# Optimization experiments

Measured on AMD Instinct MI355X. Metric: run time of the kernel, lower is better.

## Reference

```python
import jax, jax.numpy as jnp
import numpy as np

B, L, W, C = 16, 200, 64, 128
H_INTRA = 64   # intra_hidden // 2 per direction
H_INTER = 128
EPS = 1e-8


def layer_norm(x, gamma, beta):
    mu = jnp.mean(x, axis=-1, keepdims=True)
    var = jnp.mean(jnp.square(x - mu), axis=-1, keepdims=True)
    return (x - mu) * jax.lax.rsqrt(var + EPS) * gamma + beta


def gru_seq(x, Wk, Uk, b, H):
    """Keras GRU, reset_after=False, recurrent_activation=sigmoid. x: [N,T,D] -> [N,T,H]."""
    xw = jnp.einsum('ntd,dk->ntk', x, Wk) + b  # precompute input projections [N,T,3H]
    def step(h, xw_t):
        z = jax.nn.sigmoid(xw_t[:, :H] + h @ Uk[:, :H])
        r = jax.nn.sigmoid(xw_t[:, H:2 * H] + h @ Uk[:, H:2 * H])
        hh = jnp.tanh(xw_t[:, 2 * H:] + (r * h) @ Uk[:, 2 * H:])
        h = z * h + (1.0 - z) * hh
        return h, h
    h0 = jnp.zeros((x.shape[0], H), x.dtype)
    _, ys = jax.lax.scan(step, h0, jnp.swapaxes(xw, 0, 1))  # [T,N,H]
    return jnp.swapaxes(ys, 0, 1)


def skip_gru_seq(x, Wk, Uk, b, Wp, bp, H):
    """Skip-RNN GRU (Campos et al.): binary update gate u_t conditionally updates state.
    Returns (outputs [N,T,H], gates [N,T,1])."""
    xw = jnp.einsum('ntd,dk->ntk', x, Wk) + b
    def step(carry, xw_t):
        h, ut = carry
        # straight-through binarization of cumulative update prob
        u = ut + jax.lax.stop_gradient(jnp.round(ut) - ut)  # [N,1]
        z = jax.nn.sigmoid(xw_t[:, :H] + h @ Uk[:, :H])
        r = jax.nn.sigmoid(xw_t[:, H:2 * H] + h @ Uk[:, H:2 * H])
        hh = jnp.tanh(xw_t[:, 2 * H:] + (r * h) @ Uk[:, 2 * H:])
        h_new = z * h + (1.0 - z) * hh
        h = u * h_new + (1.0 - u) * h  # skip: copy state when u == 0
        delta = jax.nn.sigmoid(h @ Wp + bp)  # [N,1]
        ut_next = u * delta + (1.0 - u) * (ut + jnp.minimum(delta, 1.0 - ut))
        return (h, ut_next), (h, u)
    N = x.shape[0]
    h0 = jnp.zeros((N, H), x.dtype)
    ut0 = jnp.ones((N, 1), x.dtype)
    _, (ys, us) = jax.lax.scan(step, (h0, ut0), jnp.swapaxes(xw, 0, 1))
    return jnp.swapaxes(ys, 0, 1), jnp.swapaxes(us, 0, 1)


def setup_inputs():
    key = jax.random.key(0)
    ks = jax.random.split(key, 16)
    rn = lambda k, s: jax.random.normal(k, s, dtype=jnp.float32) * 0.05
    z = lambda s: jnp.zeros(s, jnp.float32)
    o = lambda s: jnp.ones(s, jnp.float32)
    return {
        'x': jax.random.normal(ks[0], (B, L, W, C), dtype=jnp.float32),
        'scale': jax.random.uniform(ks[1], (B, L, W, 1), dtype=jnp.float32),
        'Wf': rn(ks[2], (C, 3 * H_INTRA)), 'Uf': rn(ks[3], (H_INTRA, 3 * H_INTRA)), 'bf': z((3 * H_INTRA,)),
        'Wb': rn(ks[4], (C, 3 * H_INTRA)), 'Ub': rn(ks[5], (H_INTRA, 3 * H_INTRA)), 'bb': z((3 * H_INTRA,)),
        'W_intra_fc': rn(ks[6], (2 * H_INTRA, C)), 'b_intra_fc': z((C,)),
        'g_intra': o((C,)), 'beta_intra': z((C,)),
        'Wi': rn(ks[7], (C + 1, 3 * H_INTER)), 'Ui': rn(ks[8], (H_INTER, 3 * H_INTER)), 'bi': z((3 * H_INTER,)),
        'Wp': rn(ks[9], (H_INTER, 1)), 'bp': z((1,)),
        'W_inter_fc': rn(ks[10], (H_INTER, C)), 'b_inter_fc': z((C,)),
        'g_inter': o((C,)), 'beta_inter': z((C,)),
    }


def reference(x, scale, Wf, Uf, bf, Wb, Ub, bb, W_intra_fc, b_intra_fc, g_intra, beta_intra,
              Wi, Ui, bi, Wp, bp, W_inter_fc, b_inter_fc, g_inter, beta_inter):
    # ----- intra path: bidirectional GRU over the width axis -----
    intra_in = x.reshape(B * L, W, C)
    out_f = gru_seq(intra_in, Wf, Uf, bf, H_INTRA)
    out_b = gru_seq(intra_in[:, ::-1, :], Wb, Ub, bb, H_INTRA)[:, ::-1, :]
    intra_rnn_out = jnp.concatenate([out_f, out_b], axis=-1)  # [B*L, W, 2H]
    update_gate_intra = jnp.ones((64, L), jnp.float32)  # skip=0 branch: constant ones
    intra_dense = intra_rnn_out @ W_intra_fc + b_intra_fc  # [B*L, W, C]
    intra_out = x + layer_norm(intra_dense.reshape(B, L, W, C), g_intra, beta_intra)
    # ----- inter path: skip-GRU over the L (time) axis -----
    inter_in = jnp.transpose(intra_out, (0, 2, 1, 3)).reshape(B * W, L, C)
    scale2 = jnp.transpose(scale, (0, 2, 1, 3)).reshape(B * W, L, 1)
    inter_in = jnp.concatenate([inter_in, scale2], axis=-1)  # [B*W, L, C+1]
    inter_rnn_out, gates = skip_gru_seq(inter_in, Wi, Ui, bi, Wp, bp, H_INTER)
    update_gate_inter = gates[:, :, 0]  # [B*W, L]
    inter_dense = (inter_rnn_out @ W_inter_fc + b_inter_fc).reshape(B, W, L, C)
    inter_ln_in = jnp.transpose(inter_dense, (0, 2, 1, 3))  # [B, L, W, C]
    inter_out = intra_out + layer_norm(inter_ln_in, g_inter, beta_inter)
    return inter_out, update_gate_intra, update_gate_inter
```

## Files before the change

### kernel.cpp

```cpp
#include <hip/hip_runtime.h>
#include <cmath>


typedef float f32x16 __attribute__((ext_vector_type(16)));

__device__ __forceinline__ float sigf(float x) { return 1.0f / (1.0f + expf(-x)); }
__device__ __forceinline__ float rlanef(float v, int l) {
  return __uint_as_float(__builtin_amdgcn_readlane(__float_as_uint(v), (unsigned)l));
}
__device__ __forceinline__ void ldsbar() {
  asm volatile("s_waitcnt lgkmcnt(0)" ::: "memory");
  __builtin_amdgcn_s_barrier();
  __builtin_amdgcn_sched_barrier(0);
}

template <int SB>
__device__ __forceinline__ void macP2(const f32x16& u0, const f32x16& u1, float hv,
                                      float& a0, float& a1) {
#pragma unroll
  for (int k = 0; k < 16; ++k) {
    const float hs = rlanef(hv, SB + k);
    a0 = fmaf(u0[k], hs, a0);
    a1 = fmaf(u1[k], hs, a1);
  }
}
template <int SB>
__device__ __forceinline__ void macP1(const f32x16& u, float hv, float& a) {
#pragma unroll
  for (int k = 0; k < 16; ++k) a = fmaf(u[k], rlanef(hv, SB + k), a);
}

__global__ __launch_bounds__(256) void k_fill_ones(float* __restrict__ p, int n) {
  int i = blockIdx.x * 256 + threadIdx.x;
  if (i < n) p[i] = 1.0f;
}

enum { MA_X_FWD = 0, MA_X_BWD = 1, MA_INTER = 2 };

template <int MODE>
__global__ __launch_bounds__(256) void k_gemm_xw(
    const float* __restrict__ A0, const float* __restrict__ A1,
    const float* __restrict__ Bm, const float* __restrict__ bias,
    float* __restrict__ Cm, long M0, int N, int K, int KT)
{
  __shared__ float As[16][68];
  __shared__ float Bs[16][68];
  const int tid = threadIdx.x;
  const int tx = tid & 15, ty = tid >> 4;
  const long row0g = M0 + (long)blockIdx.x * 64;
  const int col0 = blockIdx.y * 64;
  const int lr = tid >> 2;
  const int lk4 = (tid & 3) * 4;
  const int bk = tid >> 4;
  const int bc4 = (tid & 15) * 4;
  float acc[4][4];
#pragma unroll
  for (int i = 0; i < 4; ++i)
#pragma unroll
    for (int j = 0; j < 4; ++j) acc[i][j] = 0.f;

  for (int kt = 0; kt < KT; ++kt) {
    const int k0 = kt * 16;
    {
      const long rg = row0g + lr;
      float v0, v1, v2, v3;
      if (MODE == MA_X_FWD) {
        const float4 a4 = *reinterpret_cast<const float4*>(&A0[rg * 128 + k0 + lk4]);
        v0 = a4.x; v1 = a4.y; v2 = a4.z; v3 = a4.w;
      } else if (MODE == MA_X_BWD) {
        const long s = rg >> 6; const int t = (int)(rg & 63);
        const float4 a4 =
            *reinterpret_cast<const float4*>(&A0[(s * 64 + (63 - t)) * 128 + k0 + lk4]);
        v0 = a4.x; v1 = a4.y; v2 = a4.z; v3 = a4.w;
      } else {
        const int n = (int)(rg & 1023);
        const int l = (int)(rg >> 10);
        const long rowc = ((long)(n >> 6) * 200 + l) * 64 + (n & 63);
        const long base = rowc * 128;
        if (kt < 8) {
          const float4 a4 = *reinterpret_cast<const float4*>(&A0[base + k0 + lk4]);
          v0 = a4.x; v1 = a4.y; v2 = a4.z; v3 = a4.w;
        } else {
          v0 = (lk4 == 0) ? A1[rowc] : 0.f;
          v1 = 0.f; v2 = 0.f; v3 = 0.f;
        }
      }
      As[lk4 + 0][lr] = v0;
      As[lk4 + 1][lr] = v1;
      As[lk4 + 2][lr] = v2;
      As[lk4 + 3][lr] = v3;
    }
    {
      const int k = k0 + bk;
      float4 b4 = make_float4(0.f, 0.f, 0.f, 0.f);
      if (k < K) b4 = *reinterpret_cast<const float4*>(&Bm[(long)k * N + col0 + bc4]);
      *reinterpret_cast<float4*>(&Bs[bk][bc4]) = b4;
    }
    __syncthreads();
#pragma unroll
    for (int kk = 0; kk < 16; ++kk) {
      const float4 a4 = *reinterpret_cast<const float4*>(&As[kk][ty * 4]);
      const float4 b4 = *reinterpret_cast<const float4*>(&Bs[kk][tx * 4]);
      const float av[4] = {a4.x, a4.y, a4.z, a4.w};
      const float bv[4] = {b4.x, b4.y, b4.z, b4.w};
#pragma unroll
      for (int i = 0; i < 4; ++i)
#pragma unroll
        for (int j = 0; j < 4; ++j) acc[i][j] = fmaf(av[i], bv[j], acc[i][j]);
    }
    __syncthreads();
  }
  const float4 bi4 = *reinterpret_cast<const float4*>(&bias[col0 + tx * 4]);
  const float bv[4] = {bi4.x, bi4.y, bi4.z, bi4.w};
#pragma unroll
  for (int i = 0; i < 4; ++i) {
    const long rl = (long)blockIdx.x * 64 + ty * 4 + i;
    float4 o;
    o.x = acc[i][0] + bv[0];
    o.y = acc[i][1] + bv[1];
    o.z = acc[i][2] + bv[2];
    o.w = acc[i][3] + bv[3];
    *reinterpret_cast<float4*>(&Cm[rl * (long)N + col0 + tx * 4]) = o;
  }
}

__global__ __attribute__((amdgpu_waves_per_eu(4, 4))) __launch_bounds__(256)
void k_gru_intra5(
    const float* __restrict__ xwf, const float* __restrict__ xwb,
    const float* __restrict__ Uf, const float* __restrict__ Ub,
    float* __restrict__ rnn)
{
  const int dir = blockIdx.y;
  const float* __restrict__ xw = dir ? xwb : xwf;
  const float* __restrict__ U  = dir ? Ub : Uf;
  __shared__ float h8[4][64], z8[4][64], rh8[4][64];
  __shared__ float pA[4][4][128];
  __shared__ float pB[4][4][64];
  const int tid = threadIdx.x;
  const int w = tid >> 6, lane = tid & 63;
  const long s0 = (long)blockIdx.x * 4;

  f32x16 uz, ur, uhh;
#pragma unroll
  for (int k = 0; k < 16; ++k) {
    const int row = (w * 16 + k) * 192;
    uz[k]  = U[row + lane];
    ur[k]  = U[row + 64 + lane];
    uhh[k] = U[row + 128 + lane];
  }
  h8[w][lane] = 0.f;
  __syncthreads();

  const long xrow0 = (s0 + w) * 64;
  float xa1 = xw[xrow0 * 192 + lane];
  float xa2 = xw[xrow0 * 192 + 64 + lane];
  float xb  = xw[xrow0 * 192 + 128 + lane];

  for (int t = 0; t < 64; ++t) {
    const int tn = (t < 63) ? t + 1 : t;
    const float xa1n = xw[(xrow0 + tn) * 192 + lane];
    const float xa2n = xw[(xrow0 + tn) * 192 + 64 + lane];
    const float xbn  = xw[(xrow0 + tn) * 192 + 128 + lane];
    {
      const float hv01 = h8[lane >> 5][w * 16 + (lane & 15)];
      const float hv23 = h8[2 + (lane >> 5)][w * 16 + (lane & 15)];
      float az0 = 0.f, ar0 = 0.f, az1 = 0.f, ar1 = 0.f;
      float az2 = 0.f, ar2 = 0.f, az3 = 0.f, ar3 = 0.f;
      macP2<0>(uz, ur, hv01, az0, ar0);
      macP2<32>(uz, ur, hv01, az1, ar1);
      macP2<0>(uz, ur, hv23, az2, ar2);
      macP2<32>(uz, ur, hv23, az3, ar3);
      pA[0][w][lane] = az0; pA[0][w][64 + lane] = ar0;
      pA[1][w][lane] = az1; pA[1][w][64 + lane] = ar1;
      pA[2][w][lane] = az2; pA[2][w][64 + lane] = ar2;
      pA[3][w][lane] = az3; pA[3][w][64 + lane] = ar3;
    }
    ldsbar();
    {
      const float sz = pA[w][0][lane] + pA[w][1][lane] + pA[w][2][lane] +
                       pA[w][3][lane] + xa1;
      const float sr = pA[w][0][64 + lane] + pA[w][1][64 + lane] +
                       pA[w][2][64 + lane] + pA[w][3][64 + lane] + xa2;
      z8[w][lane] = sigf(sz);
      rh8[w][lane] = sigf(sr) * h8[w][lane];
    }
    ldsbar();
    {
      const float rv01 = rh8[lane >> 5][w * 16 + (lane & 15)];
      const float rv23 = rh8[2 + (lane >> 5)][w * 16 + (lane & 15)];
      float a0 = 0.f, a1 = 0.f, a2 = 0.f, a3 = 0.f;
      macP1<0>(uhh, rv01, a0);
      macP1<32>(uhh, rv01, a1);
      macP1<0>(uhh, rv23, a2);
      macP1<32>(uhh, rv23, a3);
      pB[0][w][lane] = a0;
      pB[1][w][lane] = a1;
      pB[2][w][lane] = a2;
      pB[3][w][lane] = a3;
    }
    ldsbar();
    {
      const float pre = pB[w][0][lane] + pB[w][1][lane] + pB[w][2][lane] +
                        pB[w][3][lane] + xb;
      const float hh = tanhf(pre);
      const float z = z8[w][lane];
      const float ho = h8[w][lane];
      const float hn = z * ho + (1.f - z) * hh;
      h8[w][lane] = hn;
      const int tt = dir ? (63 - t) : t;
      rnn[((s0 + w) * 64 + tt) * 128 + dir * 64 + lane] = hn;
    }
    ldsbar();
    xa1 = xa1n; xa2 = xa2n; xb = xbn;
  }
}

__global__ __attribute__((amdgpu_waves_per_eu(4, 4))) __launch_bounds__(512)
void k_gru_inter8(
    const float* __restrict__ xw, const float* __restrict__ Ui,
    const float* __restrict__ Wp, const float* __restrict__ bp,
    float* __restrict__ rnn, float* __restrict__ gates,
    float* __restrict__ hstate, float* __restrict__ ustate,
    int t0, int nt)
{
  __shared__ float h4[2][128], z4[2][128], rh4[2][128];
  __shared__ float pA[2][8][256];
  __shared__ float pB[2][8][128];
  __shared__ float uu[2], utt[2];
  const int tid = threadIdx.x;
  const int w = tid >> 6, lane = tid & 63;
  const int kb = w << 4;
  const int n0 = blockIdx.x * 2;

  f32x16 u0, u1, u2, u3;
  f32x16 v0, v1;
#pragma unroll
  for (int k = 0; k < 16; ++k) {
    const long r = (long)(kb + k) * 384;
    u0[k] = Ui[r + lane];
    u1[k] = Ui[r + 64 + lane];
    u2[k] = Ui[r + 128 + lane];
    u3[k] = Ui[r + 192 + lane];
    v0[k] = Ui[r + 256 + lane];
    v1[k] = Ui[r + 320 + lane];
  }
  if (tid < 256) {
    const int s = tid >> 7, c = tid & 127;
    h4[s][c] = (t0 == 0) ? 0.f : hstate[(long)(n0 + s) * 128 + c];
  }
  if (tid < 2) {
    utt[tid] = (t0 == 0) ? 1.f : ustate[n0 + tid];
    uu[tid]  = (t0 == 0) ? 1.f : ustate[1024 + n0 + tid];
  }
  const float bp0 = bp[0];
  float wpA = 0.f, wpB = 0.f;
  if (w < 2) { wpA = Wp[lane]; wpB = Wp[64 + lane]; }
  __syncthreads();

  const int sC = tid >> 8;
  const int cC = tid & 255;

  for (int dl = 0; dl < nt; ++dl) {
    const float u0g = uu[0], u1g = uu[1];
    const bool act = (u0g + u1g) != 0.f;
    if (act) {
      const float xc = xw[((long)dl * 1024 + n0 + sC) * 384 + cC];
      float xbA = 0.f, xbB = 0.f;
      if (w < 2) {
        xbA = xw[((long)dl * 1024 + n0 + w) * 384 + 256 + lane];
        xbB = xw[((long)dl * 1024 + n0 + w) * 384 + 320 + lane];
      }
      {
        if (u0g != 0.f) {
          const float hv = h4[0][kb + (lane & 15)];
          float a0 = 0.f, a1 = 0.f, a2 = 0.f, a3 = 0.f;
#pragma unroll
          for (int j = 0; j < 16; ++j) {
            const float hs = rlanef(hv, j);
            a0 = fmaf(u0[j], hs, a0);
            a1 = fmaf(u1[j], hs, a1);
            a2 = fmaf(u2[j], hs, a2);
            a3 = fmaf(u3[j], hs, a3);
          }
          pA[0][w][lane] = a0; pA[0][w][64 + lane] = a1;
          pA[0][w][128 + lane] = a2; pA[0][w][192 + lane] = a3;
        }
        if (u1g != 0.f) {
          const float hv = h4[1][kb + (lane & 15)];
          float a0 = 0.f, a1 = 0.f, a2 = 0.f, a3 = 0.f;
#pragma unroll
          for (int j = 0; j < 16; ++j) {
            const float hs = rlanef(hv, j);
            a0 = fmaf(u0[j], hs, a0);
            a1 = fmaf(u1[j], hs, a1);
            a2 = fmaf(u2[j], hs, a2);
            a3 = fmaf(u3[j], hs, a3);
          }
          pA[1][w][lane] = a0; pA[1][w][64 + lane] = a1;
          pA[1][w][128 + lane] = a2; pA[1][w][192 + lane] = a3;
        }
      }
      ldsbar();
      {
        if (uu[sC] != 0.f) {
          float sum = xc;
#pragma unroll
          for (int q = 0; q < 8; ++q) sum += pA[sC][q][cC];
          if (cC < 128) z4[sC][cC] = sigf(sum);
          else rh4[sC][cC - 128] = sigf(sum) * h4[sC][cC - 128];
        }
      }
      ldsbar();
      {
        if (u0g != 0.f) {
          const float rv = rh4[0][kb + (lane & 15)];
          float b0 = 0.f, b1 = 0.f;
#pragma unroll
          for (int j = 0; j < 16; ++j) {
            const float rs = rlanef(rv, j);
            b0 = fmaf(v0[j], rs, b0);
            b1 = fmaf(v1[j], rs, b1);
          }
          pB[0][w][lane] = b0; pB[0][w][64 + lane] = b1;
        }
        if (u1g != 0.f) {
          const float rv = rh4[1][kb + (lane & 15)];
          float b0 = 0.f, b1 = 0.f;
#pragma unroll
          for (int j = 0; j < 16; ++j) {
            const float rs = rlanef(rv, j);
            b0 = fmaf(v0[j], rs, b0);
            b1 = fmaf(v1[j], rs, b1);
          }
          pB[1][w][lane] = b0; pB[1][w][64 + lane] = b1;
        }
      }
      ldsbar();
      if (w < 2) {
        const float us = uu[w];
        const float hoA = h4[w][lane], hoB = h4[w][64 + lane];
        float hqA, hqB;
        if (us != 0.f) {
          float sA = xbA, sB = xbB;
#pragma unroll
          for (int q = 0; q < 8; ++q) {
            sA += pB[w][q][lane];
            sB += pB[w][q][64 + lane];
          }
          const float hhA = tanhf(sA), hhB = tanhf(sB);
          const float zA = z4[w][lane], zB = z4[w][64 + lane];
          hqA = zA * hoA + (1.f - zA) * hhA;
          hqB = zB * hoB + (1.f - zB) * hhB;
          h4[w][lane] = hqA;
          h4[w][64 + lane] = hqB;
        } else {
          hqA = hoA; hqB = hoB;
        }
        rnn[((long)dl * 1024 + n0 + w) * 128 + lane] = hqA;
        rnn[((long)dl * 1024 + n0 + w) * 128 + 64 + lane] = hqB;
        float p = hqA * wpA + hqB * wpB;
        p += __shfl_xor(p, 32);
        p += __shfl_xor(p, 16);
        p += __shfl_xor(p, 8);
        p += __shfl_xor(p, 4);
        p += __shfl_xor(p, 2);
        p += __shfl_xor(p, 1);
        if (lane == 0) {
          const float delta = sigf(p + bp0);
          const float ut = utt[w];
          gates[(long)(n0 + w) * 200 + t0 + dl] = us;
          const float utn = us * delta + (1.f - us) * (ut + fminf(delta, 1.f - ut));
          utt[w] = utn;
          uu[w] = rintf(utn);
        }
      }
    } else {
      if (w < 2) {
        const float hqA = h4[w][lane], hqB = h4[w][64 + lane];
        rnn[((long)dl * 1024 + n0 + w) * 128 + lane] = hqA;
        rnn[((long)dl * 1024 + n0 + w) * 128 + 64 + lane] = hqB;
        float p = hqA * wpA + hqB * wpB;
        p += __shfl_xor(p, 32);
        p += __shfl_xor(p, 16);
        p += __shfl_xor(p, 8);
        p += __shfl_xor(p, 4);
        p += __shfl_xor(p, 2);
        p += __shfl_xor(p, 1);
        if (lane == 0) {
          const float delta = sigf(p + bp0);
          const float ut = utt[w];
          gates[(long)(n0 + w) * 200 + t0 + dl] = 0.f;
          const float utn = ut + fminf(delta, 1.f - ut);
          utt[w] = utn;
          uu[w] = rintf(utn);
        }
      }
    }
    ldsbar();
  }
  if (tid < 256) {
    const int s = tid >> 7, c = tid & 127;
    hstate[(long)(n0 + s) * 128 + c] = h4[s][c];
  }
  if (tid < 2) {
    ustate[n0 + tid] = utt[tid];
    ustate[1024 + n0 + tid] = uu[tid];
  }
}

template <int OM>
__global__ __launch_bounds__(256) void k_fcln(
    const float* __restrict__ A, const float* __restrict__ Wt,
    const float* __restrict__ bias, const float* __restrict__ gamma,
    const float* __restrict__ beta, const float* __restrict__ resid,
    float* __restrict__ dst, long M0)
{
  __shared__ float As[16][36];
  __shared__ float Bs[16][132];
  __shared__ float red0[32][33];
  __shared__ float red1[32][33];
  __shared__ float mu_s[32];
  __shared__ float rs_s[32];
  const int tid = threadIdx.x;
  const int tx = tid & 31, ty = tid >> 5;
  const long r0l = (long)blockIdx.x * 32;
  const int lr = tid >> 3;
  const int lk2 = (tid & 7) * 2;
  const int bkk = tid >> 4;
  const int bc8 = (tid & 15) * 8;
  float acc[4][4];
#pragma unroll
  for (int i = 0; i < 4; ++i)
#pragma unroll
    for (int j = 0; j < 4; ++j) acc[i][j] = 0.f;

  for (int kt = 0; kt < 8; ++kt) {
    const int k0 = kt * 16;
    const float2 a2 = *reinterpret_cast<const float2*>(&A[(r0l + lr) * 128 + k0 + lk2]);
    As[lk2][lr] = a2.x;
    As[lk2 + 1][lr] = a2.y;
    const float4 w0 = *reinterpret_cast<const float4*>(&Wt[(long)(k0 + bkk) * 128 + bc8]);
    const float4 w1 = *reinterpret_cast<const float4*>(&Wt[(long)(k0 + bkk) * 128 + bc8 + 4]);
    *reinterpret_cast<float4*>(&Bs[bkk][bc8]) = w0;
    *reinterpret_cast<float4*>(&Bs[bkk][bc8 + 4]) = w1;
    __syncthreads();
#pragma unroll
    for (int kk = 0; kk < 16; ++kk) {
      const float4 a4 = *reinterpret_cast<const float4*>(&As[kk][ty * 4]);
      const float4 b4 = *reinterpret_cast<const float4*>(&Bs[kk][tx * 4]);
      const float av[4] = {a4.x, a4.y, a4.z, a4.w};
      const float bv[4] = {b4.x, b4.y, b4.z, b4.w};
#pragma unroll
      for (int i = 0; i < 4; ++i)
#pragma unroll
        for (int j = 0; j < 4; ++j) acc[i][j] = fmaf(av[i], bv[j], acc[i][j]);
    }
    __syncthreads();
  }
  {
    const float4 bb4 = *reinterpret_cast<const float4*>(&bias[tx * 4]);
    const float bv[4] = {bb4.x, bb4.y, bb4.z, bb4.w};
#pragma unroll
    for (int i = 0; i < 4; ++i)
#pragma unroll
      for (int j = 0; j < 4; ++j) acc[i][j] += bv[j];
  }
#pragma unroll
  for (int i = 0; i < 4; ++i) {
    const float s = acc[i][0] + acc[i][1] + acc[i][2] + acc[i][3];
    const float q = acc[i][0] * acc[i][0] + acc[i][1] * acc[i][1] +
                    acc[i][2] * acc[i][2] + acc[i][3] * acc[i][3];
    red0[ty * 4 + i][tx] = s;
    red1[ty * 4 + i][tx] = q;
  }
  __syncthreads();
  if (tid < 32) {
    float s = 0.f, q = 0.f;
#pragma unroll
    for (int j = 0; j < 32; ++j) { s += red0[tid][j]; q += red1[tid][j]; }
    const float mu = s * (1.0f / 128.0f);
    const float var = q * (1.0f / 128.0f) - mu * mu;
    mu_s[tid] = mu;
    rs_s[tid] = 1.0f / sqrtf(var + 1e-8f);
  }
  __syncthreads();
  const float4 g4 = *reinterpret_cast<const float4*>(&gamma[tx * 4]);
  const float4 be4 = *reinterpret_cast<const float4*>(&beta[tx * 4]);
#pragma unroll
  for (int i = 0; i < 4; ++i) {
    const int rloc = ty * 4 + i;
    const long rg = M0 + r0l + rloc;
    long off;
    if (OM == 0) {
      off = rg * 128 + tx * 4;
    } else {
      const int n = (int)(rg & 1023);
      const int l = (int)(rg >> 10);
      off = (((long)(n >> 6) * 200 + l) * 64 + (n & 63)) * 128 + tx * 4;
    }
    const float4 r4 = *reinterpret_cast<const float4*>(&resid[off]);
    const float mu = mu_s[rloc], rs = rs_s[rloc];
    float4 o;
    o.x = (acc[i][0] - mu) * rs * g4.x + be4.x + r4.x;
    o.y = (acc[i][1] - mu) * rs * g4.y + be4.y + r4.y;
    o.z = (acc[i][2] - mu) * rs * g4.z + be4.z + r4.z;
    o.w = (acc[i][3] - mu) * rs * g4.w + be4.w + r4.w;
    *reinterpret_cast<float4*>(&dst[off]) = o;
  }
}

extern "C" void kernel_launch(void* const* d_in, const int* in_sizes, int n_in,
                              void* d_out, int out_size, void* d_ws, size_t ws_size,
                              hipStream_t stream)
{
  (void)in_sizes; (void)n_in; (void)out_size;
  const float* x    = (const float*)d_in[0];
  const float* scl  = (const float*)d_in[1];
  const float* Wf   = (const float*)d_in[2];
  const float* Uf   = (const float*)d_in[3];
  const float* bf   = (const float*)d_in[4];
  const float* Wb   = (const float*)d_in[5];
  const float* Ub   = (const float*)d_in[6];
  const float* bb   = (const float*)d_in[7];
  const float* Wfc1 = (const float*)d_in[8];
  const float* bfc1 = (const float*)d_in[9];
  const float* gam1 = (const float*)d_in[10];
  const float* bet1 = (const float*)d_in[11];
  const float* Wi   = (const float*)d_in[12];
  const float* Ui   = (const float*)d_in[13];
  const float* bi   = (const float*)d_in[14];
  const float* Wp   = (const float*)d_in[15];
  const float* bp   = (const float*)d_in[16];
  const float* Wfc2 = (const float*)d_in[17];
  const float* bfc2 = (const float*)d_in[18];
  const float* gam2 = (const float*)d_in[19];
  const float* bet2 = (const float*)d_in[20];

  float* outp  = (float*)d_out;
  float* io    = outp;
  float* onesp = outp + 26214400L;
  float* gates = outp + 26214400L + 12800L;
  float* ws    = (float*)d_ws;
  const long wsf = (long)(ws_size / sizeof(float));

  k_fill_ones<<<50, 256, 0, stream>>>(onesp, 12800);

  long cnI = (wsf / 32768L) & ~7L;
  if (cnI > 3200) cnI = 3200;
  if (cnI < 8) cnI = 8;
  for (long s0 = 0; s0 < 3200; s0 += cnI) {
    const long cn = (3200 - s0 < cnI) ? (3200 - s0) : cnI;
    float* xwf = ws;
    float* xwb = ws + cn * 12288L;
    float* rnn = ws + cn * 24576L;
    const long M = cn * 64;
    dim3 gg((unsigned)(M / 64), 3);
    k_gemm_xw<MA_X_FWD><<<gg, 256, 0, stream>>>(x, nullptr, Wf, bf, xwf, s0 * 64, 192, 128, 8);
    k_gemm_xw<MA_X_BWD><<<gg, 256, 0, stream>>>(x, nullptr, Wb, bb, xwb, s0 * 64, 192, 128, 8);
    dim3 gr((unsigned)(cn / 4), 2);
    k_gru_intra5<<<gr, 256, 0, stream>>>(xwf, xwb, Uf, Ub, rnn);
    k_fcln<0><<<(unsigned)(M / 32), 256, 0, stream>>>(rnn, Wfc1, bfc1, gam1, bet1, x, io, s0 * 64);
  }

  const long per_t = 1024L * 384 + 1024L * 128;
  const long state_f = 1024L * 128 + 3072L;
  long nt_alloc = (wsf - state_f) / per_t;
  if (nt_alloc > 200) nt_alloc = 200;
  if (nt_alloc < 1) nt_alloc = 1;
  float* xwi    = ws;
  float* rnnI   = ws + nt_alloc * 1024L * 384;
  float* hstate = rnnI + nt_alloc * 1024L * 128;
  float* ustate = hstate + 1024L * 128;

  for (long t0 = 0; t0 < 200; t0 += nt_alloc) {
    const int nt = (int)((200 - t0 < nt_alloc) ? (200 - t0) : nt_alloc);
    dim3 gg((unsigned)(16 * nt), 6);
    k_gemm_xw<MA_INTER><<<gg, 256, 0, stream>>>(io, scl, Wi, bi, xwi, t0 * 1024, 384, 129, 9);
    k_gru_inter8<<<512, 512, 0, stream>>>(xwi, Ui, Wp, bp, rnnI, gates, hstate, ustate,
                                          (int)t0, nt);
    k_fcln<1><<<(unsigned)(32 * nt), 256, 0, stream>>>(rnnI, Wfc2, bfc2, gam2, bet2, io, outp,
                                                       t0 * 1024);
  }
}
```

Measured before the change: 2.014 ms.

## Pack four sequences per 1024-thread block in inter GRU and prefetch inputs

The recurrent inter skip-GRU kernel now handles four sequences per block with sixteen waves, each owning an 8-row slice of the recurrent weights instead of a 16-row slice. Hidden-state values for two sequences are broadcast from one register through readlane. The next step's input projections are loaded one iteration ahead to hide global-load latency on the serial chain. In exchange, shared memory use grows a lot, the cross-wave partial-sum reductions double in length, and the grid is halved to one large block per CU.

```diff
diff --git a/kernel.cpp b/kernel.cpp
--- a/kernel.cpp
+++ b/kernel.cpp
@@ -3,6 +3,7 @@
 
 
 typedef float f32x16 __attribute__((ext_vector_type(16)));
+typedef float f32x8 __attribute__((ext_vector_type(8)));
 
 __device__ __forceinline__ float sigf(float x) { return 1.0f / (1.0f + expf(-x)); }
 __device__ __forceinline__ float rlanef(float v, int l) {
@@ -215,27 +216,27 @@
   }
 }
 
-__global__ __attribute__((amdgpu_waves_per_eu(4, 4))) __launch_bounds__(512)
-void k_gru_inter8(
+__global__ __attribute__((amdgpu_waves_per_eu(4, 4))) __launch_bounds__(1024)
+void k_gru_inter9(
     const float* __restrict__ xw, const float* __restrict__ Ui,
     const float* __restrict__ Wp, const float* __restrict__ bp,
     float* __restrict__ rnn, float* __restrict__ gates,
     float* __restrict__ hstate, float* __restrict__ ustate,
     int t0, int nt)
 {
-  __shared__ float h4[2][128], z4[2][128], rh4[2][128];
-  __shared__ float pA[2][8][256];
-  __shared__ float pB[2][8][128];
-  __shared__ float uu[2], utt[2];
+  __shared__ float h4[4][128], z4[4][128], rh4[4][128];
+  __shared__ float pA[4][16][256];
+  __shared__ float pB[4][16][128];
+  __shared__ float uu[4], utt[4];
   const int tid = threadIdx.x;
   const int w = tid >> 6, lane = tid & 63;
-  const int kb = w << 4;
-  const int n0 = blockIdx.x * 2;
-
-  f32x16 u0, u1, u2, u3;
-  f32x16 v0, v1;
-#pragma unroll
-  for (int k = 0; k < 16; ++k) {
+  const int kb = w << 3;
+  const int n0 = blockIdx.x * 4;
+
+  f32x8 u0, u1, u2, u3;
+  f32x8 v0, v1;
+#pragma unroll
+  for (int k = 0; k < 8; ++k) {
     const long r = (long)(kb + k) * 384;
     u0[k] = Ui[r + lane];
     u1[k] = Ui[r + 64 + lane];
@@ -244,60 +245,85 @@
     v0[k] = Ui[r + 256 + lane];
     v1[k] = Ui[r + 320 + lane];
   }
-  if (tid < 256) {
+  if (tid < 512) {
     const int s = tid >> 7, c = tid & 127;
     h4[s][c] = (t0 == 0) ? 0.f : hstate[(long)(n0 + s) * 128 + c];
   }
-  if (tid < 2) {
+  if (tid < 4) {
     utt[tid] = (t0 == 0) ? 1.f : ustate[n0 + tid];
     uu[tid]  = (t0 == 0) ? 1.f : ustate[1024 + n0 + tid];
   }
   const float bp0 = bp[0];
   float wpA = 0.f, wpB = 0.f;
-  if (w < 2) { wpA = Wp[lane]; wpB = Wp[64 + lane]; }
+  if (w < 4) { wpA = Wp[lane]; wpB = Wp[64 + lane]; }
   __syncthreads();
 
   const int sC = tid >> 8;
   const int cC = tid & 255;
+  float xc = xw[(long)(n0 + sC) * 384 + cC];
+  float xbA = 0.f, xbB = 0.f;
+  if (w < 4) {
+    xbA = xw[(long)(n0 + w) * 384 + 256 + lane];
+    xbB = xw[(long)(n0 + w) * 384 + 320 + lane];
+  }
 
   for (int dl = 0; dl < nt; ++dl) {
-    const float u0g = uu[0], u1g = uu[1];
-    const bool act = (u0g + u1g) != 0.f;
+    const float u0g = uu[0], u1g = uu[1], u2g = uu[2], u3g = uu[3];
+    const bool act = (u0g + u1g + u2g + u3g) != 0.f;
+    const int dn = (dl + 1 < nt) ? dl + 1 : dl;
+    const float xcn = xw[((long)dn * 1024 + n0 + sC) * 384 + cC];
+    float xbAn = 0.f, xbBn = 0.f;
+    if (w < 4) {
+      xbAn = xw[((long)dn * 1024 + n0 + w) * 384 + 256 + lane];
+      xbBn = xw[((long)dn * 1024 + n0 + w) * 384 + 320 + lane];
+    }
     if (act) {
-      const float xc = xw[((long)dl * 1024 + n0 + sC) * 384 + cC];
-      float xbA = 0.f, xbB = 0.f;
-      if (w < 2) {
-        xbA = xw[((long)dl * 1024 + n0 + w) * 384 + 256 + lane];
-        xbB = xw[((long)dl * 1024 + n0 + w) * 384 + 320 + lane];
-      }
       {
+        const float hv01 = h4[lane >> 5][kb + (lane & 7)];
+        const float hv23 = h4[2 + (lane >> 5)][kb + (lane & 7)];
         if (u0g != 0.f) {
-          const float hv = h4[0][kb + (lane & 15)];
           float a0 = 0.f, a1 = 0.f, a2 = 0.f, a3 = 0.f;
 #pragma unroll
-          for (int j = 0; j < 16; ++j) {
-            const float hs = rlanef(hv, j);
-            a0 = fmaf(u0[j], hs, a0);
-            a1 = fmaf(u1[j], hs, a1);
-            a2 = fmaf(u2[j], hs, a2);
-            a3 = fmaf(u3[j], hs, a3);
+          for (int k = 0; k < 8; ++k) {
+            const float hs = rlanef(hv01, k);
+            a0 = fmaf(u0[k], hs, a0); a1 = fmaf(u1[k], hs, a1);
+            a2 = fmaf(u2[k], hs, a2); a3 = fmaf(u3[k], hs, a3);
           }
           pA[0][w][lane] = a0; pA[0][w][64 + lane] = a1;
           pA[0][w][128 + lane] = a2; pA[0][w][192 + lane] = a3;
         }
         if (u1g != 0.f) {
-          const float hv = h4[1][kb + (lane & 15)];
           float a0 = 0.f, a1 = 0.f, a2 = 0.f, a3 = 0.f;
 #pragma unroll
-          for (int j = 0; j < 16; ++j) {
-            const float hs = rlanef(hv, j);
-            a0 = fmaf(u0[j], hs, a0);
-            a1 = fmaf(u1[j], hs, a1);
-            a2 = fmaf(u2[j], hs, a2);
-            a3 = fmaf(u3[j], hs, a3);
+          for (int k = 0; k < 8; ++k) {
+            const float hs = rlanef(hv01, 32 + k);
+            a0 = fmaf(u0[k], hs, a0); a1 = fmaf(u1[k], hs, a1);
+            a2 = fmaf(u2[k], hs, a2); a3 = fmaf(u3[k], hs, a3);
           }
           pA[1][w][lane] = a0; pA[1][w][64 + lane] = a1;
           pA[1][w][128 + lane] = a2; pA[1][w][192 + lane] = a3;
+        }
+        if (u2g != 0.f) {
+          float a0 = 0.f, a1 = 0.f, a2 = 0.f, a3 = 0.f;
+#pragma unroll
+          for (int k = 0; k < 8; ++k) {
+            const float hs = rlanef(hv23, k);
+            a0 = fmaf(u0[k], hs, a0); a1 = fmaf(u1[k], hs, a1);
+            a2 = fmaf(u2[k], hs, a2); a3 = fmaf(u3[k], hs, a3);
+          }
+          pA[2][w][lane] = a0; pA[2][w][64 + lane] = a1;
+          pA[2][w][128 + lane] = a2; pA[2][w][192 + lane] = a3;
+        }
+        if (u3g != 0.f) {
+          float a0 = 0.f, a1 = 0.f, a2 = 0.f, a3 = 0.f;
+#pragma unroll
+          for (int k = 0; k < 8; ++k) {
+            const float hs = rlanef(hv23, 32 + k);
+            a0 = fmaf(u0[k], hs, a0); a1 = fmaf(u1[k], hs, a1);
+            a2 = fmaf(u2[k], hs, a2); a3 = fmaf(u3[k], hs, a3);
+          }
+          pA[3][w][lane] = a0; pA[3][w][64 + lane] = a1;
+          pA[3][w][128 + lane] = a2; pA[3][w][192 + lane] = a3;
         }
       }
       ldsbar();
@@ -305,45 +331,61 @@
         if (uu[sC] != 0.f) {
           float sum = xc;
 #pragma unroll
-          for (int q = 0; q < 8; ++q) sum += pA[sC][q][cC];
+          for (int q = 0; q < 16; ++q) sum += pA[sC][q][cC];
           if (cC < 128) z4[sC][cC] = sigf(sum);
           else rh4[sC][cC - 128] = sigf(sum) * h4[sC][cC - 128];
         }
       }
       ldsbar();
       {
+        const float rv01 = rh4[lane >> 5][kb + (lane & 7)];
+        const float rv23 = rh4[2 + (lane >> 5)][kb + (lane & 7)];
         if (u0g != 0.f) {
-          const float rv = rh4[0][kb + (lane & 15)];
           float b0 = 0.f, b1 = 0.f;
 #pragma unroll
-          for (int j = 0; j < 16; ++j) {
-            const float rs = rlanef(rv, j);
-            b0 = fmaf(v0[j], rs, b0);
-            b1 = fmaf(v1[j], rs, b1);
+          for (int k = 0; k < 8; ++k) {
+            const float rs = rlanef(rv01, k);
+            b0 = fmaf(v0[k], rs, b0); b1 = fmaf(v1[k], rs, b1);
           }
           pB[0][w][lane] = b0; pB[0][w][64 + lane] = b1;
         }
         if (u1g != 0.f) {
-          const float rv = rh4[1][kb + (lane & 15)];
           float b0 = 0.f, b1 = 0.f;
 #pragma unroll
-          for (int j = 0; j < 16; ++j) {
-            const float rs = rlanef(rv, j);
-            b0 = fmaf(v0[j], rs, b0);
-            b1 = fmaf(v1[j], rs, b1);
+          for (int k = 0; k < 8; ++k) {
+            const float rs = rlanef(rv01, 32 + k);
+            b0 = fmaf(v0[k], rs, b0); b1 = fmaf(v1[k], rs, b1);
           }
           pB[1][w][lane] = b0; pB[1][w][64 + lane] = b1;
+        }
+        if (u2g != 0.f) {
+          float b0 = 0.f, b1 = 0.f;
+#pragma unroll
+          for (int k = 0; k < 8; ++k) {
+            const float rs = rlanef(rv23, k);
+            b0 = fmaf(v0[k], rs, b0); b1 = fmaf(v1[k], rs, b1);
+          }
+          pB[2][w][lane] = b0; pB[2][w][64 + lane] = b1;
+        }
+        if (u3g != 0.f) {
+          float b0 = 0.f, b1 = 0.f;
+#pragma unroll
+          for (int k = 0; k < 8; ++k) {
+            const float rs = rlanef(rv23, 32 + k);
+            b0 = fmaf(v0[k], rs, b0); b1 = fmaf(v1[k], rs, b1);
+          }
+          pB[3][w][lane] = b0; pB[3][w][64 + lane] = b1;
         }
       }
       ldsbar();
-      if (w < 2) {
+      if (w < 4) {
         const float us = uu[w];
         const float hoA = h4[w][lane], hoB = h4[w][64 + lane];
         float hqA, hqB;
         if (us != 0.f) {
           float sA = xbA, sB = xbB;
 #pragma unroll
-          for (int q = 0; q < 8; ++q) {
+          for (int q = 0; q < 16; ++q) {
             sA += pB[w][q][lane];
             sB += pB[w][q][64 + lane];
           }
@@ -375,7 +417,7 @@
         }
       }
     } else {
-      if (w < 2) {
+      if (w < 4) {
         const float hqA = h4[w][lane], hqB = h4[w][64 + lane];
         rnn[((long)dl * 1024 + n0 + w) * 128 + lane] = hqA;
         rnn[((long)dl * 1024 + n0 + w) * 128 + 64 + lane] = hqB;
@@ -397,12 +439,13 @@
       }
     }
     ldsbar();
-  }
-  if (tid < 256) {
+    xc = xcn; xbA = xbAn; xbB = xbBn;
+  }
+  if (tid < 512) {
     const int s = tid >> 7, c = tid & 127;
     hstate[(long)(n0 + s) * 128 + c] = h4[s][c];
   }
-  if (tid < 2) {
+  if (tid < 4) {
     ustate[n0 + tid] = utt[tid];
     ustate[1024 + n0 + tid] = uu[tid];
   }
@@ -576,8 +619,8 @@
     const int nt = (int)((200 - t0 < nt_alloc) ? (200 - t0) : nt_alloc);
     dim3 gg((unsigned)(16 * nt), 6);
     k_gemm_xw<MA_INTER><<<gg, 256, 0, stream>>>(io, scl, Wi, bi, xwi, t0 * 1024, 384, 129, 9);
-    k_gru_inter8<<<512, 512, 0, stream>>>(xwi, Ui, Wp, bp, rnnI, gates, hstate, ustate,
-                                          (int)t0, nt);
+    k_gru_inter9<<<256, 1024, 0, stream>>>(xwi, Ui, Wp, bp, rnnI, gates, hstate, ustate,
+                                           (int)t0, nt);
     k_fcln<1><<<(unsigned)(32 * nt), 256, 0, stream>>>(rnnI, Wfc2, bfc2, gam2, bet2, io, outp,
                                                        t0 * 1024);
   }
```

Result: faster. 1.791 ms (-11.1%).
